# Performance work log

Hardware: AMD Instinct MI355X
Metric: run time of the kernel (lower is better)

## Reference

```python
import jax, jax.numpy as jnp
import numpy as np

N = 50000        # nodes
E = 1_600_000    # edges
G = 64           # graphs in batch
IN = 10          # raw node feature width
XS, XE = 4, 10   # bus slice -> in_dim = 6
H = 256          # hidden_dim
OUT = 256        # out_dim
L = 3            # n_layers per expert
NE = 8           # n_experts
K = 2            # top_k


def _w(key, shape):
    fan_in = shape[-2] if len(shape) > 1 else shape[-1]
    return jax.random.normal(key, shape, jnp.float32) / np.sqrt(fan_in).astype(np.float32)


def setup_inputs() -> dict:
    key = jax.random.key(0)
    ks = jax.random.split(key, 18)
    x = jax.random.normal(ks[0], (N, IN), jnp.float32)
    edge_index = jax.random.randint(ks[1], (2, E), 0, N, dtype=jnp.int32)
    batch = jnp.sort(jax.random.randint(ks[2], (N,), 0, G, dtype=jnp.int32))
    return {
        "x": x,
        "edge_index": edge_index,
        "batch": batch,
        # SharedBusEncoder: Linear(in_dim, hidden) + ReLU
        "W_enc": _w(ks[3], (XE - XS, H)), "b_enc": jnp.zeros((H,), jnp.float32),
        # semantic BaseRouter: Linear(H,H)+ReLU+Linear(H,NE)
        "Ws1": _w(ks[4], (H, H)), "bs1": jnp.zeros((H,), jnp.float32),
        "Ws2": _w(ks[5], (H, NE)), "bs2": jnp.zeros((NE,), jnp.float32),
        # structural BaseRouter: Linear(2,H)+ReLU+Linear(H,NE)
        "Wt1": _w(ks[6], (2, H)), "bt1": jnp.zeros((H,), jnp.float32),
        "Wt2": _w(ks[7], (H, NE)), "bt2": jnp.zeros((NE,), jnp.float32),
        # GraphConvExpert stacks: x' = x@W_self + (sum_neighbors x)@W_neigh + b
        "W_self": _w(ks[8], (NE, L, H, OUT)),
        "W_neigh": _w(ks[9], (NE, L, H, OUT)),
        "b_exp": jnp.zeros((NE, L, OUT), jnp.float32),
    }


def reference(x, edge_index, batch, W_enc, b_enc, Ws1, bs1, Ws2, bs2,
              Wt1, bt1, Wt2, bt2, W_self, W_neigh, b_exp):
    src, dst = edge_index[0], edge_index[1]

    # SharedBusEncoder on bus feature slice
    h = jax.nn.relu(x[:, XS:XE] @ W_enc + b_enc)                       # [N, H]

    # graph_size_features: per-graph log node/edge counts, broadcast to nodes
    nodes_per_g = jax.ops.segment_sum(jnp.ones((N,), jnp.float32), batch, G)
    edges_per_g = jax.ops.segment_sum(jnp.ones((E,), jnp.float32), batch[src], G)
    size_feat = jnp.stack([jnp.log1p(nodes_per_g), jnp.log1p(edges_per_g)], -1)[batch]  # [N, 2]

    # dual routers, averaged
    sem = jax.nn.relu(h @ Ws1 + bs1) @ Ws2 + bs2                       # [N, NE]
    stru = jax.nn.relu(size_feat @ Wt1 + bt1) @ Wt2 + bt2              # [N, NE]
    logits = 0.5 * sem + 0.5 * stru

    # sparse_routing: softmax -> top-k mask -> renormalize (eval path, no noise)
    probs = jax.nn.softmax(logits, axis=-1)
    _, topi = jax.lax.top_k(probs, K)                                  # [N, K]
    mask = jnp.zeros_like(probs).at[jnp.arange(N)[:, None], topi].set(1.0)
    sp = probs * mask
    sparse = sp / jnp.sum(sp, axis=-1, keepdims=True)                  # [N, NE]

    # dense GraphConv experts over all nodes
    def run_expert(Ws, Wn, b):
        z = h
        for l in range(L):
            agg = jax.ops.segment_sum(z[src], dst, N)                  # neighbor sum
            z = z @ Ws[l] + agg @ Wn[l] + b[l]
            if l < L - 1:
                z = jax.nn.relu(z)
        return z                                                        # [N, OUT]

    y = jax.vmap(run_expert)(W_self, W_neigh, b_exp)                   # [NE, N, OUT]
    return jnp.einsum('end,ne->nd', y, sparse)                         # [N, OUT]
```

## Files before the change

kernel.cpp:

```cpp
#include <hip/hip_runtime.h>
#include <hip/hip_bf16.h>


#define NN 50000
#define EE 1600000
#define GG 64
#define HH 256
#define NEXP 8
#define LAY 3
#define KD 512
#define MT 128

typedef __attribute__((ext_vector_type(8))) short bf16x8;
typedef __attribute__((ext_vector_type(8))) unsigned short u16x8;
typedef __attribute__((ext_vector_type(4))) float f32x4;

__device__ __forceinline__ float bf2f(unsigned short u) {
    union { unsigned int i; float f; } v; v.i = ((unsigned int)u) << 16; return v.f;
}
__device__ __forceinline__ unsigned short f2bf(float f) {
    union { unsigned int i; float f; } v; v.f = f;
    unsigned int r = (v.i + 0x7FFFu + ((v.i >> 16) & 1u)) >> 16;
    return (unsigned short)r;
}
__device__ __forceinline__ void async_cp16(const unsigned short* g, unsigned short* l) {
    __builtin_amdgcn_global_load_lds(
        (const __attribute__((address_space(1))) unsigned int*)g,
        (__attribute__((address_space(3))) unsigned int*)l, 16, 0, 0);
}

__global__ void encoder_kernel(const float* __restrict__ x, const float* __restrict__ W,
                               const float* __restrict__ b, unsigned short* __restrict__ out) {
    int n = blockIdx.x, j = threadIdx.x;
    float acc = b[j];
#pragma unroll
    for (int i = 0; i < 6; i++) acc += x[n * 10 + 4 + i] * W[i * HH + j];
    acc = fmaxf(acc, 0.f);
    out[(long)n * KD + j] = f2bf(acc);
}

__global__ void pack_experts(const float* __restrict__ Wself, const float* __restrict__ Wneigh,
                             unsigned short* __restrict__ Bt) {
    int idx = blockIdx.x * 256 + threadIdx.x;
    int n = idx & 255; int r = idx >> 8;
    int k = r & 511; int el = r >> 9;
    float v = (k < 256) ? Wself[((el * 256) + k) * 256 + n]
                        : Wneigh[((el * 256) + (k - 256)) * 256 + n];
    int kt = k >> 6, kk = (k >> 5) & 1, q = (k >> 3) & 3, j = k & 7;
    int ct = n >> 4, mm = n & 15, lane = q * 16 + mm;
    Bt[(size_t)el * 131072 + (size_t)(kt * 32 + ct * 2 + kk) * 512 + lane * 8 + j] = f2bf(v);
}

__global__ void pack_ws1(const float* __restrict__ W, unsigned short* __restrict__ Bt) {
    int idx = blockIdx.x * 256 + threadIdx.x;
    int n = idx & 255; int k = idx >> 8;
    int kt = k >> 6, kk = (k >> 5) & 1, q = (k >> 3) & 3, j = k & 7;
    int ct = n >> 4, mm = n & 15, lane = q * 16 + mm;
    Bt[(size_t)(kt * 32 + ct * 2 + kk) * 512 + lane * 8 + j] = f2bf(W[k * HH + n]);
}

__global__ void deg_kernel(const int* __restrict__ src, const int* __restrict__ dst,
                           int* __restrict__ deg, int* __restrict__ outdeg) {
    int e = blockIdx.x * 256 + threadIdx.x;
    if (e < EE) {
        atomicAdd(&deg[dst[e]], 1);
        atomicAdd(&outdeg[src[e]], 1);
    }
}

__global__ void hist_kernel(const int* __restrict__ batch, const int* __restrict__ outdeg,
                            int* __restrict__ ncnt, int* __restrict__ ecnt) {
    __shared__ int hn[GG], he[GG];
    if (threadIdx.x < GG) { hn[threadIdx.x] = 0; he[threadIdx.x] = 0; }
    __syncthreads();
    int i = blockIdx.x * 256 + threadIdx.x;
    if (i < NN) {
        int g = batch[i];
        atomicAdd(&hn[g], 1);
        atomicAdd(&he[g], outdeg[i]);
    }
    __syncthreads();
    if (threadIdx.x < GG) {
        if (hn[threadIdx.x]) atomicAdd(&ncnt[threadIdx.x], hn[threadIdx.x]);
        if (he[threadIdx.x]) atomicAdd(&ecnt[threadIdx.x], he[threadIdx.x]);
    }
}

__global__ void stru_kernel(const int* __restrict__ ncnt, const int* __restrict__ ecnt,
                            const float* __restrict__ Wt1, const float* __restrict__ bt1,
                            const float* __restrict__ Wt2, const float* __restrict__ bt2,
                            float* __restrict__ strug) {
    __shared__ float t[HH];
    int g = blockIdx.x, j = threadIdx.x;
    float nf = log1pf((float)ncnt[g]);
    float ef = log1pf((float)ecnt[g]);
    float v = nf * Wt1[j] + ef * Wt1[HH + j] + bt1[j];
    t[j] = fmaxf(v, 0.f);
    __syncthreads();
    if (j < 8) {
        float sum = bt2[j];
        for (int k = 0; k < HH; k++) sum += t[k] * Wt2[k * 8 + j];
        strug[g * 8 + j] = sum;
    }
}

__global__ void scan_kernel(const int* __restrict__ deg, int* __restrict__ rowstart,
                            int* __restrict__ cursor) {
    __shared__ int wsum[16];
    __shared__ int carry_s;
    int tid = threadIdx.x;
    int wid = tid >> 6, lane = tid & 63;
    if (tid == 0) carry_s = 0;
    __syncthreads();
    for (int base = 0; base < NN; base += 1024) {
        int i = base + tid;
        int v = (i < NN) ? deg[i] : 0;
        int sc = v;
#pragma unroll
        for (int off = 1; off < 64; off <<= 1) {
            int t = __shfl_up(sc, off, 64);
            if (lane >= off) sc += t;
        }
        if (lane == 63) wsum[wid] = sc;
        __syncthreads();
        int carry = carry_s;
        int prev = 0;
        for (int w = 0; w < wid; w++) prev += wsum[w];
        int excl = carry + prev + sc - v;
        if (i < NN) { rowstart[i] = excl; cursor[i] = excl; }
        __syncthreads();
        if (tid == 1023) carry_s = carry + prev + sc;
    }
    __syncthreads();
    if (tid == 0) rowstart[NN] = carry_s;
}

__global__ void scatter_kernel(const int* __restrict__ src, const int* __restrict__ dst,
                               int* __restrict__ cursor, unsigned short* __restrict__ cols) {
    int e = blockIdx.x * 256 + threadIdx.x;
    if (e < EE) {
        int p = atomicAdd(&cursor[dst[e]], 1);
        cols[p] = (unsigned short)src[e];
    }
}

__global__ void agg_kernel(const unsigned short* __restrict__ Z, unsigned short* __restrict__ Aout,
                           const int* __restrict__ rowstart, const unsigned short* __restrict__ cols,
                           const int* __restrict__ list, const int* __restrict__ cntp) {
    int half = threadIdx.x >> 5;
    int lane = threadIdx.x & 31;
    int idx = blockIdx.x * 8 + half;
    int limit = cntp ? *cntp : NN;
    if (idx >= limit) return;
    int nid = list ? list[idx] : idx;
    int s = rowstart[nid], e = rowstart[nid + 1];
    float acc[8] = {0.f, 0.f, 0.f, 0.f, 0.f, 0.f, 0.f, 0.f};
    int i = s;
    for (; i + 8 <= e; i += 8) {
        int c[8];
#pragma unroll
        for (int u = 0; u < 8; u++) c[u] = (int)cols[i + u];
        u16x8 v[8];
#pragma unroll
        for (int u = 0; u < 8; u++) v[u] = *(const u16x8*)&Z[(long)c[u] * KD + lane * 8];
#pragma unroll
        for (int u = 0; u < 8; u++)
#pragma unroll
            for (int j = 0; j < 8; j++) acc[j] += bf2f(v[u][j]);
    }
    for (; i < e; i++) {
        int c = (int)cols[i];
        u16x8 v = *(const u16x8*)&Z[(long)c * KD + lane * 8];
#pragma unroll
        for (int j = 0; j < 8; j++) acc[j] += bf2f(v[j]);
    }
    u16x8 o;
#pragma unroll
    for (int j = 0; j < 8; j++) o[j] = f2bf(acc[j]);
    *(u16x8*)&Aout[(long)nid * KD + 256 + lane * 8] = o;
}

__global__ void route_kernel(const unsigned short* __restrict__ T, const float* __restrict__ Ws2,
                             const float* __restrict__ bs2, const float* __restrict__ strug,
                             const int* __restrict__ batch, float* __restrict__ sparse) {
    int nid = blockIdx.x * 4 + (threadIdx.x >> 6);
    if (nid >= NN) return;
    int lane = threadIdx.x & 63;
    float s[8];
#pragma unroll
    for (int j = 0; j < 8; j++) s[j] = 0.f;
    ushort4 t4 = *(const ushort4*)&T[(long)nid * HH + lane * 4];
    float tv[4] = { bf2f(t4.x), bf2f(t4.y), bf2f(t4.z), bf2f(t4.w) };
#pragma unroll
    for (int kk = 0; kk < 4; kk++) {
        int k = lane * 4 + kk;
#pragma unroll
        for (int j = 0; j < 8; j++) s[j] += tv[kk] * Ws2[k * 8 + j];
    }
#pragma unroll
    for (int off = 32; off >= 1; off >>= 1) {
#pragma unroll
        for (int j = 0; j < 8; j++) s[j] += __shfl_xor(s[j], off, 64);
    }
    int g = batch[nid];
    float p[8], mx = -1e30f;
#pragma unroll
    for (int j = 0; j < 8; j++) {
        p[j] = 0.5f * (s[j] + bs2[j] + strug[g * 8 + j]);
        mx = fmaxf(mx, p[j]);
    }
    float ex[8];
#pragma unroll
    for (int j = 0; j < 8; j++) ex[j] = expf(p[j] - mx);
    int i1 = 0;
#pragma unroll
    for (int j = 1; j < 8; j++) if (ex[j] > ex[i1]) i1 = j;
    int i2 = (i1 == 0) ? 1 : 0;
#pragma unroll
    for (int j = 0; j < 8; j++) if (j != i1 && ex[j] > ex[i2]) i2 = j;
    float r = 1.f / (ex[i1] + ex[i2]);
    if (lane < 8)
        sparse[(long)nid * 8 + lane] = (lane == i1) ? ex[i1] * r : (lane == i2) ? ex[i2] * r : 0.f;
}

__global__ void build_lists(const float* __restrict__ sparse, int* __restrict__ cnt,
                            int* __restrict__ lists) {
    int n = blockIdx.x * 256 + threadIdx.x;
    if (n >= NN) return;
#pragma unroll
    for (int e = 0; e < NEXP; e++) {
        if (sparse[n * 8 + e] > 0.f) {
            int p = atomicAdd(&cnt[e], 1);
            lists[(long)e * NN + p] = n;
        }
    }
}

template <int MODE>
__global__ __launch_bounds__(256, 2) void gemm_kernel(
    const unsigned short* __restrict__ A, int lda, int K,
    const unsigned short* __restrict__ Bt, const float* __restrict__ bias,
    void* __restrict__ outp, int ldz,
    const float* __restrict__ sparse, int expert,
    const int* __restrict__ list, const int* __restrict__ cntp) {
    __shared__ __align__(16) unsigned short Blds[2][16384];
    __shared__ int nodeids[MT];
    const int tid = threadIdx.x;
    const int wave = tid >> 6, lane = tid & 63;
    const int wr = wave & 1, wc = wave >> 1;
    const int m = lane & 15, q = lane >> 4;
    const int row0 = blockIdx.x * MT;
    const int NT = K >> 6;

    if constexpr (MODE == 1) {
        int limit = *cntp;
        if (row0 >= limit) return;
        if (tid < MT) {
            int rr = row0 + tid;
            nodeids[tid] = (rr < limit) ? list[rr] : -1;
        }
    }

    {
        const unsigned short* g = Bt + (size_t)wave * 4096 + lane * 8;
        unsigned short* l = &Blds[0][wave * 4096];
#pragma unroll
        for (int i = 0; i < 8; i++) async_cp16(g + i * 512, l + i * 512);
    }
    if constexpr (MODE == 1) __syncthreads();

    int arow[4];
#pragma unroll
    for (int rt = 0; rt < 4; rt++) {
        int rr = wr * 64 + rt * 16 + m;
        if constexpr (MODE == 0) {
            int gr = row0 + rr;
            arow[rt] = (gr < NN) ? gr : NN - 1;
        } else {
            int nid2 = nodeids[rr];
            arow[rt] = (nid2 >= 0) ? nid2 : 0;
        }
    }

    f32x4 acc[4][8];
#pragma unroll
    for (int i = 0; i < 4; i++)
#pragma unroll
        for (int j = 0; j < 8; j++) acc[i][j] = (f32x4){0.f, 0.f, 0.f, 0.f};

    for (int kt = 0; kt < NT; kt++) {
        __syncthreads();
        if (kt + 1 < NT) {
            const unsigned short* g = Bt + (size_t)(kt + 1) * 16384 + wave * 4096 + lane * 8;
            unsigned short* l = &Blds[(kt + 1) & 1][wave * 4096];
#pragma unroll
            for (int i = 0; i < 8; i++) async_cp16(g + i * 512, l + i * 512);
        }
        bf16x8 afr[4][2];
#pragma unroll
        for (int rt = 0; rt < 4; rt++)
#pragma unroll
            for (int kk = 0; kk < 2; kk++)
                afr[rt][kk] = *(const bf16x8*)&A[(size_t)arow[rt] * lda + kt * 64 + kk * 32 + q * 8];
        const unsigned short* bb = Blds[kt & 1];
#pragma unroll
        for (int kk = 0; kk < 2; kk++)
#pragma unroll
            for (int ct = 0; ct < 8; ct++) {
                bf16x8 bfr = *(const bf16x8*)&bb[(size_t)((wc * 8 + ct) * 2 + kk) * 512 + lane * 8];
#pragma unroll
                for (int rt = 0; rt < 4; rt++)
                    acc[rt][ct] = __builtin_amdgcn_mfma_f32_16x16x32_bf16(afr[rt][kk], bfr,
                                                                          acc[rt][ct], 0, 0, 0);
            }
    }

#pragma unroll
    for (int rt = 0; rt < 4; rt++) {
        int rr0 = wr * 64 + rt * 16 + q * 4;
        if constexpr (MODE == 0) {
#pragma unroll
            for (int ct = 0; ct < 8; ct++) {
                int col = wc * 128 + ct * 16 + m;
                float bv = bias[col];
#pragma unroll
                for (int r = 0; r < 4; r++) {
                    int grow = row0 + rr0 + r;
                    if (grow < NN) {
                        float v = fmaxf(acc[rt][ct][r] + bv, 0.f);
                        ((unsigned short*)outp)[(size_t)grow * ldz + col] = f2bf(v);
                    }
                }
            }
        } else {
            int nid4[4]; float w4[4];
#pragma unroll
            for (int r = 0; r < 4; r++) {
                nid4[r] = nodeids[rr0 + r];
                w4[r] = (nid4[r] >= 0) ? sparse[(size_t)nid4[r] * 8 + expert] : 0.f;
            }
#pragma unroll
            for (int ct = 0; ct < 8; ct++) {
                int col = wc * 128 + ct * 16 + m;
                float bv = bias[col];
#pragma unroll
                for (int r = 0; r < 4; r++) {
                    if (nid4[r] >= 0) {
                        float* o = (float*)outp + (size_t)nid4[r] * HH + col;
                        *o += w4[r] * (acc[rt][ct][r] + bv);
                    }
                }
            }
        }
    }
}

extern "C" void kernel_launch(void* const* d_in, const int* in_sizes, int n_in,
                              void* d_out, int out_size, void* d_ws, size_t ws_size,
                              hipStream_t stream) {
    const float* x     = (const float*)d_in[0];
    const int*   ei    = (const int*)d_in[1];
    const int*   src   = ei;
    const int*   dst   = ei + EE;
    const int*   batch = (const int*)d_in[2];
    const float* W_enc = (const float*)d_in[3];
    const float* b_enc = (const float*)d_in[4];
    const float* Ws1   = (const float*)d_in[5];
    const float* bs1   = (const float*)d_in[6];
    const float* Ws2   = (const float*)d_in[7];
    const float* bs2   = (const float*)d_in[8];
    const float* Wt1   = (const float*)d_in[9];
    const float* bt1   = (const float*)d_in[10];
    const float* Wt2   = (const float*)d_in[11];
    const float* bt2   = (const float*)d_in[12];
    const float* W_self  = (const float*)d_in[13];
    const float* W_neigh = (const float*)d_in[14];
    const float* b_exp   = (const float*)d_in[15];
    float* out = (float*)d_out;

    char* ws = (char*)d_ws;
    size_t off = 0;
    auto alloc = [&](size_t b) { size_t p = off; off = (off + b + 255) & ~(size_t)255; return p; };
    const size_t MPAD = 50048;

    unsigned short* Ash = (unsigned short*)(ws + alloc(MPAD * KD * 2));
    unsigned short* Ab0 = (unsigned short*)(ws + alloc(MPAD * KD * 2));
    unsigned short* Ab1 = (unsigned short*)(ws + alloc(MPAD * KD * 2));
    unsigned short* Tbuf = Ab1;
    unsigned short* BtE = (unsigned short*)(ws + alloc((size_t)NEXP * LAY * HH * KD * 2));
    unsigned short* Bt1 = (unsigned short*)(ws + alloc((size_t)HH * HH * 2));
    float* sparse  = (float*)(ws + alloc((size_t)NN * 8 * 4));
    float* strug   = (float*)(ws + alloc((size_t)GG * 8 * 4));
    int* ncnt      = (int*)(ws + alloc((size_t)GG * 4));
    int* ecnt      = (int*)(ws + alloc((size_t)GG * 4));
    int* deg       = (int*)(ws + alloc((size_t)NN * 4));
    int* outdeg    = (int*)(ws + alloc((size_t)NN * 4));
    int* rowstart  = (int*)(ws + alloc((size_t)(NN + 1) * 4));
    int* cursor    = (int*)(ws + alloc((size_t)NN * 4));
    unsigned short* cols = (unsigned short*)(ws + alloc((size_t)EE * 2));
    int* lists     = (int*)(ws + alloc((size_t)NEXP * NN * 4));
    int* cnt8      = (int*)(ws + alloc((size_t)NEXP * 4));

    hipMemsetAsync(ncnt, 0, GG * 4, stream);
    hipMemsetAsync(ecnt, 0, GG * 4, stream);
    hipMemsetAsync(deg, 0, (size_t)NN * 4, stream);
    hipMemsetAsync(outdeg, 0, (size_t)NN * 4, stream);
    hipMemsetAsync(cnt8, 0, NEXP * 4, stream);
    hipMemsetAsync(out, 0, (size_t)NN * HH * 4, stream);

    pack_experts<<<NEXP * LAY * KD * HH / 256, 256, 0, stream>>>(W_self, W_neigh, BtE);
    pack_ws1<<<HH * HH / 256, 256, 0, stream>>>(Ws1, Bt1);
    encoder_kernel<<<NN, HH, 0, stream>>>(x, W_enc, b_enc, Ash);

    deg_kernel<<<(EE + 255) / 256, 256, 0, stream>>>(src, dst, deg, outdeg);
    hist_kernel<<<(NN + 255) / 256, 256, 0, stream>>>(batch, outdeg, ncnt, ecnt);
    scan_kernel<<<1, 1024, 0, stream>>>(deg, rowstart, cursor);
    scatter_kernel<<<(EE + 255) / 256, 256, 0, stream>>>(src, dst, cursor, cols);
    stru_kernel<<<GG, HH, 0, stream>>>(ncnt, ecnt, Wt1, bt1, Wt2, bt2, strug);

    const int GB = (NN + MT - 1) / MT;
    const int AGB = NN / 8;

    gemm_kernel<0><<<GB, 256, 0, stream>>>(Ash, KD, HH, Bt1, bs1, Tbuf, HH, nullptr, 0,
                                           nullptr, nullptr);
    route_kernel<<<(NN + 3) / 4, 256, 0, stream>>>(Tbuf, Ws2, bs2, strug, batch, sparse);
    build_lists<<<(NN + 255) / 256, 256, 0, stream>>>(sparse, cnt8, lists);

    agg_kernel<<<AGB, 256, 0, stream>>>(Ash, Ash, rowstart, cols, nullptr, nullptr);

    for (int e = 0; e < NEXP; e++) {
        const unsigned short* B0 = BtE + (size_t)(e * LAY + 0) * 131072;
        const unsigned short* B1 = BtE + (size_t)(e * LAY + 1) * 131072;
        const unsigned short* B2 = BtE + (size_t)(e * LAY + 2) * 131072;
        const float* bb = b_exp + (size_t)e * LAY * HH;
        const int* le = lists + (size_t)e * NN;
        gemm_kernel<0><<<GB, 256, 0, stream>>>(Ash, KD, KD, B0, bb, Ab0, KD, nullptr, 0,
                                               nullptr, nullptr);
        agg_kernel<<<AGB, 256, 0, stream>>>(Ab0, Ab0, rowstart, cols, nullptr, nullptr);
        gemm_kernel<0><<<GB, 256, 0, stream>>>(Ab0, KD, KD, B1, bb + HH, Ab1, KD, nullptr, 0,
                                               nullptr, nullptr);
        agg_kernel<<<AGB, 256, 0, stream>>>(Ab1, Ab1, rowstart, cols, le, cnt8 + e);
        gemm_kernel<1><<<GB, 256, 0, stream>>>(Ab1, KD, KD, B2, bb + 2 * HH, out, 0, sparse, e,
                                               le, cnt8 + e);
    }
}
```

Baseline: 2.477 ms.

## Drop LDS staging in GEMM, read B from global, halve row tile

The GEMM kernel no longer stages B tiles in LDS through async global-to-LDS copies with double buffering. Each wave now reads its B fragments straight from global memory, relying on L2 and cache, and software-prefetches the next A fragments into registers. The row tile shrinks from 128 to 64, the K loop becomes a compile-time template parameter so it fully unrolls, and launch bounds rise to 3 blocks per CU for more occupancy. The cost is more global and L2 traffic for B, since each block re-reads it without LDS sharing across waves, plus twice as many blocks.

```diff
diff --git a/kernel.cpp b/kernel.cpp
--- a/kernel.cpp
+++ b/kernel.cpp
@@ -9,7 +9,7 @@
 #define NEXP 8
 #define LAY 3
 #define KD 512
-#define MT 128
+#define MT 64
 
 typedef __attribute__((ext_vector_type(8))) short bf16x8;
 typedef __attribute__((ext_vector_type(8))) unsigned short u16x8;
@@ -22,11 +22,6 @@
     union { unsigned int i; float f; } v; v.f = f;
     unsigned int r = (v.i + 0x7FFFu + ((v.i >> 16) & 1u)) >> 16;
     return (unsigned short)r;
-}
-__device__ __forceinline__ void async_cp16(const unsigned short* g, unsigned short* l) {
-    __builtin_amdgcn_global_load_lds(
-        (const __attribute__((address_space(1))) unsigned int*)g,
-        (__attribute__((address_space(3))) unsigned int*)l, 16, 0, 0);
 }
 
 __global__ void encoder_kernel(const float* __restrict__ x, const float* __restrict__ W,
@@ -236,21 +231,19 @@
     }
 }
 
-template <int MODE>
-__global__ __launch_bounds__(256, 2) void gemm_kernel(
-    const unsigned short* __restrict__ A, int lda, int K,
+template <int MODE, int KT>
+__global__ __launch_bounds__(256, 3) void gemm_kernel(
+    const unsigned short* __restrict__ A, int lda,
     const unsigned short* __restrict__ Bt, const float* __restrict__ bias,
     void* __restrict__ outp, int ldz,
     const float* __restrict__ sparse, int expert,
     const int* __restrict__ list, const int* __restrict__ cntp) {
-    __shared__ __align__(16) unsigned short Blds[2][16384];
     __shared__ int nodeids[MT];
     const int tid = threadIdx.x;
     const int wave = tid >> 6, lane = tid & 63;
     const int wr = wave & 1, wc = wave >> 1;
     const int m = lane & 15, q = lane >> 4;
     const int row0 = blockIdx.x * MT;
-    const int NT = K >> 6;
 
     if constexpr (MODE == 1) {
         int limit = *cntp;
@@ -259,65 +252,72 @@
             int rr = row0 + tid;
             nodeids[tid] = (rr < limit) ? list[rr] : -1;
         }
-    }
-
-    {
-        const unsigned short* g = Bt + (size_t)wave * 4096 + lane * 8;
-        unsigned short* l = &Blds[0][wave * 4096];
-#pragma unroll
-        for (int i = 0; i < 8; i++) async_cp16(g + i * 512, l + i * 512);
-    }
-    if constexpr (MODE == 1) __syncthreads();
-
-    int arow[4];
-#pragma unroll
-    for (int rt = 0; rt < 4; rt++) {
-        int rr = wr * 64 + rt * 16 + m;
+        __syncthreads();
+    }
+
+    const unsigned short* aptr[2];
+#pragma unroll
+    for (int rt = 0; rt < 2; rt++) {
+        int rr = wr * 32 + rt * 16 + m;
+        int ar;
         if constexpr (MODE == 0) {
             int gr = row0 + rr;
-            arow[rt] = (gr < NN) ? gr : NN - 1;
+            ar = (gr < NN) ? gr : NN - 1;
         } else {
             int nid2 = nodeids[rr];
-            arow[rt] = (nid2 >= 0) ? nid2 : 0;
-        }
-    }
-
-    f32x4 acc[4][8];
-#pragma unroll
-    for (int i = 0; i < 4; i++)
+            ar = (nid2 >= 0) ? nid2 : 0;
+        }
+        aptr[rt] = A + (size_t)ar * lda + q * 8;
+    }
+
+    f32x4 acc[2][8];
+#pragma unroll
+    for (int i = 0; i < 2; i++)
 #pragma unroll
         for (int j = 0; j < 8; j++) acc[i][j] = (f32x4){0.f, 0.f, 0.f, 0.f};
 
-    for (int kt = 0; kt < NT; kt++) {
-        __syncthreads();
-        if (kt + 1 < NT) {
-            const unsigned short* g = Bt + (size_t)(kt + 1) * 16384 + wave * 4096 + lane * 8;
-            unsigned short* l = &Blds[(kt + 1) & 1][wave * 4096];
-#pragma unroll
-            for (int i = 0; i < 8; i++) async_cp16(g + i * 512, l + i * 512);
-        }
-        bf16x8 afr[4][2];
-#pragma unroll
-        for (int rt = 0; rt < 4; rt++)
-#pragma unroll
-            for (int kk = 0; kk < 2; kk++)
-                afr[rt][kk] = *(const bf16x8*)&A[(size_t)arow[rt] * lda + kt * 64 + kk * 32 + q * 8];
-        const unsigned short* bb = Blds[kt & 1];
+    bf16x8 a_cur[2][2];
+#pragma unroll
+    for (int rt = 0; rt < 2; rt++)
 #pragma unroll
         for (int kk = 0; kk < 2; kk++)
-#pragma unroll
-            for (int ct = 0; ct < 8; ct++) {
-                bf16x8 bfr = *(const bf16x8*)&bb[(size_t)((wc * 8 + ct) * 2 + kk) * 512 + lane * 8];
-#pragma unroll
-                for (int rt = 0; rt < 4; rt++)
-                    acc[rt][ct] = __builtin_amdgcn_mfma_f32_16x16x32_bf16(afr[rt][kk], bfr,
+            a_cur[rt][kk] = *(const bf16x8*)(aptr[rt] + kk * 32);
+
+    const unsigned short* bp = Bt + (size_t)(wc * 8) * 2 * 512 + lane * 8;
+
+#pragma unroll
+    for (int kt = 0; kt < KT; kt++) {
+        bf16x8 a_nxt[2][2];
+        if (kt + 1 < KT) {
+#pragma unroll
+            for (int rt = 0; rt < 2; rt++)
+#pragma unroll
+                for (int kk = 0; kk < 2; kk++)
+                    a_nxt[rt][kk] = *(const bf16x8*)(aptr[rt] + (kt + 1) * 64 + kk * 32);
+        }
+        const unsigned short* bb = bp + (size_t)kt * 16384;
+#pragma unroll
+        for (int kk = 0; kk < 2; kk++) {
+            bf16x8 bfr[8];
+#pragma unroll
+            for (int ct = 0; ct < 8; ct++)
+                bfr[ct] = *(const bf16x8*)&bb[(size_t)(ct * 2 + kk) * 512];
+#pragma unroll
+            for (int ct = 0; ct < 8; ct++)
+#pragma unroll
+                for (int rt = 0; rt < 2; rt++)
+                    acc[rt][ct] = __builtin_amdgcn_mfma_f32_16x16x32_bf16(a_cur[rt][kk], bfr[ct],
                                                                           acc[rt][ct], 0, 0, 0);
-            }
-    }
-
-#pragma unroll
-    for (int rt = 0; rt < 4; rt++) {
-        int rr0 = wr * 64 + rt * 16 + q * 4;
+        }
+#pragma unroll
+        for (int rt = 0; rt < 2; rt++)
+#pragma unroll
+            for (int kk = 0; kk < 2; kk++) a_cur[rt][kk] = a_nxt[rt][kk];
+    }
+
+#pragma unroll
+    for (int rt = 0; rt < 2; rt++) {
+        int rr0 = wr * 32 + rt * 16 + q * 4;
         if constexpr (MODE == 0) {
 #pragma unroll
             for (int ct = 0; ct < 8; ct++) {
@@ -421,8 +421,8 @@
     const int GB = (NN + MT - 1) / MT;
     const int AGB = NN / 8;
 
-    gemm_kernel<0><<<GB, 256, 0, stream>>>(Ash, KD, HH, Bt1, bs1, Tbuf, HH, nullptr, 0,
-                                           nullptr, nullptr);
+    gemm_kernel<0, 4><<<GB, 256, 0, stream>>>(Ash, KD, Bt1, bs1, Tbuf, HH, nullptr, 0,
+                                              nullptr, nullptr);
     route_kernel<<<(NN + 3) / 4, 256, 0, stream>>>(Tbuf, Ws2, bs2, strug, batch, sparse);
     build_lists<<<(NN + 255) / 256, 256, 0, stream>>>(sparse, cnt8, lists);
 
@@ -434,13 +434,13 @@
         const unsigned short* B2 = BtE + (size_t)(e * LAY + 2) * 131072;
         const float* bb = b_exp + (size_t)e * LAY * HH;
         const int* le = lists + (size_t)e * NN;
-        gemm_kernel<0><<<GB, 256, 0, stream>>>(Ash, KD, KD, B0, bb, Ab0, KD, nullptr, 0,
-                                               nullptr, nullptr);
+        gemm_kernel<0, 8><<<GB, 256, 0, stream>>>(Ash, KD, B0, bb, Ab0, KD, nullptr, 0,
+                                                  nullptr, nullptr);
         agg_kernel<<<AGB, 256, 0, stream>>>(Ab0, Ab0, rowstart, cols, nullptr, nullptr);
-        gemm_kernel<0><<<GB, 256, 0, stream>>>(Ab0, KD, KD, B1, bb + HH, Ab1, KD, nullptr, 0,
-                                               nullptr, nullptr);
+        gemm_kernel<0, 8><<<GB, 256, 0, stream>>>(Ab0, KD, B1, bb + HH, Ab1, KD, nullptr, 0,
+                                                  nullptr, nullptr);
         agg_kernel<<<AGB, 256, 0, stream>>>(Ab1, Ab1, rowstart, cols, le, cnt8 + e);
-        gemm_kernel<1><<<GB, 256, 0, stream>>>(Ab1, KD, KD, B2, bb + 2 * HH, out, 0, sparse, e,
-                                               le, cnt8 + e);
-    }
-}
+        gemm_kernel<1, 8><<<GB, 256, 0, stream>>>(Ab1, KD, B2, bb + 2 * HH, out, 0, sparse, e,
+                                                  le, cnt8 + e);
+    }
+}
```

New measurement: 2.831 ms. +14.3%, slower.
